# Kernel optimization log

Hardware: AMD Instinct MI355X
Metric: run time of the kernel (lower is better)

Reference implementation:

```python
import jax, jax.numpy as jnp
import numpy as np

B = 65536   # batch
S = 3       # pad_size / seq len
DIN = 72    # input feature dim
D = 100     # dim_model
H = 10      # num_head
DH = D // H # dim_head = 10
FF = 512    # ffn hidden
L = 8       # encoder layers
CLS = 40    # cls_dim


def _pos_encoding():
    pe = np.array([[pos / 10000.0 ** (i // 2 * 2.0 / D) for i in range(D)]
                   for pos in range(S)], dtype=np.float32)
    pe[:, 0::2] = np.sin(pe[:, 0::2])
    pe[:, 1::2] = np.cos(pe[:, 1::2])
    return jnp.asarray(pe)  # [S, D]


def setup_inputs() -> dict:
    key = jax.random.key(0)
    ks = jax.random.split(key, 24)
    n = lambda k, shape: 0.05 * jax.random.normal(k, shape, dtype=jnp.float32)
    inp = {
        'x': jax.random.normal(ks[0], (B, S, DIN), dtype=jnp.float32),
        'label': jax.random.randint(ks[1], (B,), 0, CLS),
        'fa_label': jax.random.randint(ks[2], (B,), 0, CLS),
        'We': n(ks[3], (D, DIN)), 'be': n(ks[4], (D,)),
        'pe': _pos_encoding(),
        'Wq': n(ks[5], (L, D, D)), 'bq': n(ks[6], (L, D)),
        'Wk': n(ks[7], (L, D, D)), 'bk': n(ks[8], (L, D)),
        'Wv': n(ks[9], (L, D, D)), 'bv': n(ks[10], (L, D)),
        'Wo': n(ks[11], (L, D, D)), 'bo': n(ks[12], (L, D)),
        'ln1_g': jnp.ones((L, D), jnp.float32), 'ln1_b': jnp.zeros((L, D), jnp.float32),
        'W1': n(ks[13], (L, FF, D)), 'b1': n(ks[14], (L, FF)),
        'W2': n(ks[15], (L, D, FF)), 'b2': n(ks[16], (L, D)),
        'ln2_g': jnp.ones((L, D), jnp.float32), 'ln2_b': jnp.zeros((L, D), jnp.float32),
        'Wf': n(ks[17], (CLS, S * D)), 'bf': n(ks[18], (CLS,)),
    }
    return inp


def _ln(x, g, b, eps=1e-5):
    m = x.mean(-1, keepdims=True)
    v = ((x - m) ** 2).mean(-1, keepdims=True)
    return (x - m) / jnp.sqrt(v + eps) * g + b


def _forward(x, We, be, pe, Wq, bq, Wk, bk, Wv, bv, Wo, bo,
             ln1_g, ln1_b, W1, b1, W2, b2, ln2_g, ln2_b, Wf, bf):
    Bsz = x.shape[0]
    out = x @ We.T + be          # [B, S, D] embedding
    out = out + pe               # positional encoding (dropout = identity in eval)
    scale = DH ** -0.5
    for i in range(L):
        xin = out
        Q = xin @ Wq[i].T + bq[i]
        K = xin @ Wk[i].T + bk[i]
        V = xin @ Wv[i].T + bv[i]
        # Faithful row-major reshape (original uses .view, which interleaves
        # seq and head dims rather than a transpose-based head split).
        Qh = Q.reshape(Bsz * H, -1, DH)   # [B*H, S, DH]
        Kh = K.reshape(Bsz * H, -1, DH)
        Vh = V.reshape(Bsz * H, -1, DH)
        attn = jax.nn.softmax(jnp.einsum('bqd,bkd->bqk', Qh, Kh) * scale, axis=-1)
        ctx = jnp.einsum('bqk,bkd->bqd', attn, Vh).reshape(Bsz, -1, D)
        out = _ln(ctx @ Wo[i].T + bo[i] + xin, ln1_g[i], ln1_b[i])
        # position-wise FFN
        h = jax.nn.relu(out @ W1[i].T + b1[i])
        out = _ln(h @ W2[i].T + b2[i] + out, ln2_g[i], ln2_b[i])
    out = out.reshape(Bsz, S * D) @ Wf.T + bf   # [B, CLS]
    return out


def reference(x, label, fa_label, We, be, pe, Wq, bq, Wk, bk, Wv, bv, Wo, bo,
              ln1_g, ln1_b, W1, b1, W2, b2, ln2_g, ln2_b, Wf, bf):
    # label / fa_label are unused in the original forward
    return _forward(x, We, be, pe, Wq, bq, Wk, bk, Wv, bv, Wo, bo,
                    ln1_g, ln1_b, W1, b1, W2, b2, ln2_g, ln2_b, Wf, bf)
```

## Files before the change

kernel.cpp:

```cpp
#include <hip/hip_runtime.h>
#include <hip/hip_bf16.h>


typedef __attribute__((ext_vector_type(8))) short short8;
typedef __attribute__((ext_vector_type(4))) float floatx4;

namespace {
constexpr int S = 3, DIN = 72, D = 100, FF = 512, L = 8, CLS = 40;
constexpr int NB = 16, R = 48, NT = 256;
constexpr int LDA = 136;
constexpr int LDH = 200;
constexpr float SCALE = 0.3162277660168379f;

constexpr int PL_QKVO = 7 * 4 * 512;
constexpr int WQ_OFF = 0;
constexpr int WK_OFF = WQ_OFF + L * PL_QKVO;
constexpr int WV_OFF = WK_OFF + L * PL_QKVO;
constexpr int WO_OFF = WV_OFF + L * PL_QKVO;
constexpr int PL_W1 = 32 * 4 * 512;
constexpr int W1_OFF = WO_OFF + L * PL_QKVO;
constexpr int PL_W2 = 7 * 16 * 512;
constexpr int W2_OFF = W1_OFF + L * PL_W1;
constexpr int WE_OFF = W2_OFF + L * PL_W2;
}

__device__ __forceinline__ unsigned short f2bf(float f) {
  unsigned int u = __float_as_uint(f);
  u = u + 0x7fffu + ((u >> 16) & 1u);
  return (unsigned short)(u >> 16);
}

__device__ __forceinline__ unsigned pkbf(float a, float b) {
  __hip_bfloat162 h = __float22bfloat162_rn(make_float2(a, b));
  return *reinterpret_cast<unsigned*>(&h);
}

__device__ __forceinline__ void st_bf4(unsigned short* p, floatx4 v) {
  *reinterpret_cast<uint2*>(p) = make_uint2(pkbf(v.x, v.y), pkbf(v.z, v.w));
}

__device__ __forceinline__ void load10(float* o, const unsigned short* p) {
  const unsigned* u = (const unsigned*)p;
#pragma unroll
  for (int w = 0; w < 5; ++w) {
    unsigned x = u[w];
    o[2 * w] = __uint_as_float(x << 16);
    o[2 * w + 1] = __uint_as_float(x & 0xffff0000u);
  }
}

__device__ __forceinline__ void ldwf4(const unsigned short* base, short8* o) {
#pragma unroll
  for (int ks = 0; ks < 4; ++ks) o[ks] = *(const short8*)(base + ks * 512);
}

__device__ __forceinline__ void ln_rows(float* xrow, const float* srow,
                                        const float* __restrict__ g,
                                        const float* __restrict__ b,
                                        unsigned short* sArow, int ln,
                                        int cnt) {
  floatx4 v[7];
  float sum = 0.f;
#pragma unroll
  for (int i = 0; i < 7; ++i)
    if (i < cnt) {
      const int col = i * 16 + ln * 4;
      floatx4 t = *(const floatx4*)(xrow + col) + *(const floatx4*)(srow + col);
      v[i] = t;
      sum += t.x + t.y + t.z + t.w;
    }
  sum += __shfl_xor(sum, 1, 4);
  sum += __shfl_xor(sum, 2, 4);
  const float mean = sum * 0.01f;
  float var = 0.f;
#pragma unroll
  for (int i = 0; i < 7; ++i)
    if (i < cnt) {
      floatx4 d = v[i] - mean;
      var += d.x * d.x + d.y * d.y + d.z * d.z + d.w * d.w;
    }
  var += __shfl_xor(var, 1, 4);
  var += __shfl_xor(var, 2, 4);
  const float rstd = rsqrtf(var * 0.01f + 1e-5f);
#pragma unroll
  for (int i = 0; i < 7; ++i)
    if (i < cnt) {
      const int col = i * 16 + ln * 4;
      floatx4 o = (v[i] - mean) * rstd * *(const floatx4*)(g + col) +
                  *(const floatx4*)(b + col);
      *(floatx4*)(xrow + col) = o;
      st_bf4(sArow + col, o);
    }
}

__global__ void prep_weights(const float* __restrict__ Wq, const float* __restrict__ Wk,
                             const float* __restrict__ Wv, const float* __restrict__ Wo,
                             const float* __restrict__ W1, const float* __restrict__ W2,
                             const float* __restrict__ We,
                             unsigned short* __restrict__ ws) {
  const int gid = blockIdx.x * 256 + threadIdx.x;
  constexpr int T_QKVO = 8 * 7 * 4 * 64;
  constexpr int T_W1 = 8 * 32 * 4 * 64;
  constexpr int T_W2 = 8 * 7 * 16 * 64;
  constexpr int T_WE = 7 * 3 * 64;
  if (gid >= 4 * T_QKVO + T_W1 + T_W2 + T_WE) return;

  const float* src;
  unsigned short* dst;
  int within, ntc, ksc, N, Ksrc, lstride;
  if (gid < 4 * T_QKVO) {
    const int t = gid / T_QKVO;
    within = gid % T_QKVO;
    src = (t == 0 ? Wq : t == 1 ? Wk : t == 2 ? Wv : Wo);
    dst = ws + (t == 0 ? WQ_OFF : t == 1 ? WK_OFF : t == 2 ? WV_OFF : WO_OFF);
    ntc = 7; ksc = 4; N = 100; Ksrc = 100; lstride = 10000;
  } else if (gid < 4 * T_QKVO + T_W1) {
    within = gid - 4 * T_QKVO;
    src = W1; dst = ws + W1_OFF;
    ntc = 32; ksc = 4; N = 512; Ksrc = 100; lstride = 51200;
  } else if (gid < 4 * T_QKVO + T_W1 + T_W2) {
    within = gid - 4 * T_QKVO - T_W1;
    src = W2; dst = ws + W2_OFF;
    ntc = 7; ksc = 16; N = 100; Ksrc = 512; lstride = 51200;
  } else {
    within = gid - 4 * T_QKVO - T_W1 - T_W2;
    src = We; dst = ws + WE_OFF;
    ntc = 7; ksc = 3; N = 100; Ksrc = 72; lstride = 0;
  }
  const int lane = within & 63;
  int tmp = within >> 6;
  const int ks = tmp % ksc; tmp /= ksc;
  const int nt = tmp % ntc;
  const int lay = tmp / ntc;
  const int n = nt * 16 + (lane & 15);
  const int kb = ks * 32 + (lane >> 4) * 8;
  const float* sp = src + (size_t)lay * lstride + (size_t)n * Ksrc;
  unsigned short o[8];
#pragma unroll
  for (int j = 0; j < 8; ++j) {
    const int k = kb + j;
    float v = (n < N && k < Ksrc) ? sp[k] : 0.f;
    o[j] = f2bf(v);
  }
  uint4 pk = make_uint4((unsigned)o[0] | ((unsigned)o[1] << 16),
                        (unsigned)o[2] | ((unsigned)o[3] << 16),
                        (unsigned)o[4] | ((unsigned)o[5] << 16),
                        (unsigned)o[6] | ((unsigned)o[7] << 16));
  *reinterpret_cast<uint4*>(dst + (size_t)within * 8) = pk;
}

__global__ __launch_bounds__(NT, 3)
void geomap_mfma(const float* __restrict__ gx,
                 const float* __restrict__ be, const float* __restrict__ pe,
                 const float* __restrict__ bq, const float* __restrict__ bk,
                 const float* __restrict__ bv, const float* __restrict__ bo,
                 const float* __restrict__ g1, const float* __restrict__ bt1,
                 const float* __restrict__ b1, const float* __restrict__ b2,
                 const float* __restrict__ g2, const float* __restrict__ bt2,
                 const float* __restrict__ Wf, const float* __restrict__ bfc,
                 const unsigned short* __restrict__ ws,
                 float* __restrict__ gout) {
  __shared__ __align__(16) char smem[51456];
  unsigned short* sA = (unsigned short*)smem;
  float* sXf = (float*)(smem + 13056);
  unsigned short* sQ = (unsigned short*)(smem + 32256);
  unsigned short* sK = (unsigned short*)(smem + 41856);
  float* scr = (float*)(smem + 32256);
  unsigned short* sH = (unsigned short*)(smem + 32256);

  const int tid = threadIdx.x;
  const int lane = tid & 63;
  const int wid = tid >> 6;
  const int l15 = lane & 15;
  const int quad = lane >> 4;
  const int blk = blockIdx.x;

  const int row_o = tid >> 2, ln_o = tid & 3;
  const int cnt_o = (ln_o == 0) ? 7 : 6;

  for (int i = tid; i < R * LDA / 2; i += NT) ((unsigned*)sA)[i] = 0u;
  __syncthreads();
  for (int i = tid; i < R * DIN / 2; i += NT) {
    const int row = i / 36, c = (i % 36) * 2;
    const float2 f2 = *(const float2*)(gx + ((size_t)blk * R + row) * DIN + c);
    ((unsigned*)sA)[row * (LDA / 2) + (c >> 1)] = pkbf(f2.x, f2.y);
  }
  __syncthreads();

  {
    short8 xe[3][3];
#pragma unroll
    for (int mt = 0; mt < 3; ++mt)
#pragma unroll
      for (int ks = 0; ks < 3; ++ks)
        xe[mt][ks] = *(const short8*)(sA + (mt * 16 + l15) * LDA + ks * 32 + quad * 8);
    __syncthreads();
    for (int nt = wid; nt < 7; nt += 4) {
      const unsigned short* wb = ws + WE_OFF + (size_t)(nt * 3) * 512 + (size_t)lane * 8;
      short8 w0 = *(const short8*)(wb);
      short8 w1 = *(const short8*)(wb + 512);
      short8 w2 = *(const short8*)(wb + 1024);
      const int n0 = nt * 16 + quad * 4;
      floatx4 a[3];
#pragma unroll
      for (int mt = 0; mt < 3; ++mt) {
        a[mt] = floatx4{0.f, 0.f, 0.f, 0.f};
        a[mt] = __builtin_amdgcn_mfma_f32_16x16x32_bf16(w0, xe[mt][0], a[mt], 0, 0, 0);
        a[mt] = __builtin_amdgcn_mfma_f32_16x16x32_bf16(w1, xe[mt][1], a[mt], 0, 0, 0);
        a[mt] = __builtin_amdgcn_mfma_f32_16x16x32_bf16(w2, xe[mt][2], a[mt], 0, 0, 0);
      }
      if (n0 < D) {
        const floatx4 bev = *(const floatx4*)(be + n0);
#pragma unroll
        for (int mt = 0; mt < 3; ++mt) {
          const int row = mt * 16 + l15;
          const int s = row % 3;
          const floatx4 pev = *(const floatx4*)(pe + s * D + n0);
          const floatx4 o = a[mt] + bev + pev;
          *(floatx4*)(sXf + row * D + n0) = o;
          st_bf4(sA + row * LDA + n0, o);
        }
      }
    }
  }
  __syncthreads();

  for (int lay = 0; lay < L; ++lay) {
    {
      short8 xf[3][4];
#pragma unroll
      for (int mt = 0; mt < 3; ++mt)
#pragma unroll
        for (int ks = 0; ks < 4; ++ks)
          xf[mt][ks] = *(const short8*)(sA + (mt * 16 + l15) * LDA + ks * 32 + quad * 8);
      __syncthreads();
      const unsigned short* wbase[3] = {ws + WQ_OFF + lay * PL_QKVO,
                                        ws + WK_OFF + lay * PL_QKVO,
                                        ws + WV_OFF + lay * PL_QKVO};
      for (int u = wid; u < 21; u += 4) {
        const int mat = u / 7, nt = u % 7;
        short8 wf[4];
        ldwf4(wbase[mat] + (size_t)nt * 2048 + (size_t)lane * 8, wf);
        const int n0 = nt * 16 + quad * 4;
        floatx4 bias = {0.f, 0.f, 0.f, 0.f};
        const float* bsrc = (mat == 0 ? bq : mat == 1 ? bk : bv) + lay * D;
        if (n0 < D) bias = *(const floatx4*)(bsrc + n0);
        floatx4 a0 = bias, a1 = bias, a2 = bias;
#pragma unroll
        for (int ks = 0; ks < 4; ++ks) {
          a0 = __builtin_amdgcn_mfma_f32_16x16x32_bf16(wf[ks], xf[0][ks], a0, 0, 0, 0);
          a1 = __builtin_amdgcn_mfma_f32_16x16x32_bf16(wf[ks], xf[1][ks], a1, 0, 0, 0);
          a2 = __builtin_amdgcn_mfma_f32_16x16x32_bf16(wf[ks], xf[2][ks], a2, 0, 0, 0);
        }
        if (n0 < D) {
          const floatx4 av[3] = {a0, a1, a2};
#pragma unroll
          for (int mt = 0; mt < 3; ++mt) {
            const int row = mt * 16 + l15;
            if (mat == 0) st_bf4(sQ + row * 100 + n0, av[mt]);
            else if (mat == 1) st_bf4(sK + row * 100 + n0, av[mt]);
            else st_bf4(sA + row * LDA + n0, av[mt]);
          }
        }
      }
    }
    __syncthreads();

    if (tid < 160) {
      const int e = tid / 10, h = tid % 10;
      const unsigned short* Qe = sQ + e * 300;
      const unsigned short* Ke = sK + e * 300;
      float Kv[3][10];
#pragma unroll
      for (int t = 0; t < 3; ++t) load10(Kv[t], Ke + h * 30 + t * 10);
      float p[3][3];
#pragma unroll
      for (int sq = 0; sq < 3; ++sq) {
        float q[10];
        load10(q, Qe + h * 30 + sq * 10);
        float sc[3];
#pragma unroll
        for (int t = 0; t < 3; ++t) {
          float s0 = 0.f;
#pragma unroll
          for (int j = 0; j < 10; ++j) s0 += q[j] * Kv[t][j];
          sc[t] = s0 * SCALE;
        }
        const float m = fmaxf(sc[0], fmaxf(sc[1], sc[2]));
        float p0 = __expf(sc[0] - m), p1 = __expf(sc[1] - m), p2 = __expf(sc[2] - m);
        const float inv = 1.f / (p0 + p1 + p2);
        p[sq][0] = p0 * inv; p[sq][1] = p1 * inv; p[sq][2] = p2 * inv;
      }
      float ctx[3][10];
#pragma unroll
      for (int sq = 0; sq < 3; ++sq)
#pragma unroll
        for (int j = 0; j < 10; ++j) ctx[sq][j] = 0.f;
#pragma unroll
      for (int t = 0; t < 3; ++t) {
        const int pv = h * 30 + t * 10;
        float vv[10];
        load10(vv, sA + (e * 3 + pv / 100) * LDA + (pv % 100));
#pragma unroll
        for (int sq = 0; sq < 3; ++sq)
#pragma unroll
          for (int j = 0; j < 10; ++j) ctx[sq][j] += p[sq][t] * vv[j];
      }
#pragma unroll
      for (int sq = 0; sq < 3; ++sq) {
        const int pq = h * 30 + sq * 10;
        unsigned* dp = (unsigned*)(sA + (e * 3 + pq / 100) * LDA + (pq % 100));
#pragma unroll
        for (int w = 0; w < 5; ++w)
          dp[w] = pkbf(ctx[sq][2 * w], ctx[sq][2 * w + 1]);
      }
    }
    __syncthreads();

    {
      short8 cf[3][4];
#pragma unroll
      for (int mt = 0; mt < 3; ++mt)
#pragma unroll
        for (int ks = 0; ks < 4; ++ks)
          cf[mt][ks] = *(const short8*)(sA + (mt * 16 + l15) * LDA + ks * 32 + quad * 8);
      const unsigned short* wbase = ws + WO_OFF + lay * PL_QKVO;
      for (int u = wid; u < 7; u += 4) {
        short8 wf[4];
        ldwf4(wbase + (size_t)u * 2048 + (size_t)lane * 8, wf);
        const int n0 = u * 16 + quad * 4;
        floatx4 bias = {0.f, 0.f, 0.f, 0.f};
        if (n0 < D) bias = *(const floatx4*)(bo + lay * D + n0);
        floatx4 a0 = bias, a1 = bias, a2 = bias;
#pragma unroll
        for (int ks = 0; ks < 4; ++ks) {
          a0 = __builtin_amdgcn_mfma_f32_16x16x32_bf16(wf[ks], cf[0][ks], a0, 0, 0, 0);
          a1 = __builtin_amdgcn_mfma_f32_16x16x32_bf16(wf[ks], cf[1][ks], a1, 0, 0, 0);
          a2 = __builtin_amdgcn_mfma_f32_16x16x32_bf16(wf[ks], cf[2][ks], a2, 0, 0, 0);
        }
        if (n0 < D) {
          const floatx4 av[3] = {a0, a1, a2};
#pragma unroll
          for (int mt = 0; mt < 3; ++mt)
            *(floatx4*)(scr + (mt * 16 + l15) * D + n0) = av[mt];
        }
      }
    }
    __syncthreads();
    if (tid < 192)
      ln_rows(sXf + row_o * D, scr + row_o * D, g1 + lay * D, bt1 + lay * D,
              sA + row_o * LDA, ln_o, cnt_o);
    __syncthreads();

    {
      short8 ff[3][4];
#pragma unroll
      for (int mt = 0; mt < 3; ++mt)
#pragma unroll
        for (int ks = 0; ks < 4; ++ks)
          ff[mt][ks] = *(const short8*)(sA + (mt * 16 + l15) * LDA + ks * 32 + quad * 8);
      floatx4 facc[2][3];
      const int ntA = wid, ntB = wid + 4;
#pragma unroll
      for (int idx = 0; idx < 2; ++idx) {
        const int nt = idx == 0 ? ntA : ntB;
        const int n0 = nt * 16 + quad * 4;
        floatx4 bias = {0.f, 0.f, 0.f, 0.f};
        if (nt < 7 && n0 < D) bias = *(const floatx4*)(b2 + lay * D + n0);
#pragma unroll
        for (int mt = 0; mt < 3; ++mt) facc[idx][mt] = bias;
      }
      const unsigned short* w1b = ws + W1_OFF + (size_t)lay * PL_W1;
      const unsigned short* w2b = ws + W2_OFF + (size_t)lay * PL_W2;

#pragma unroll
      for (int c = 0; c < 3; ++c) {
        const int base_nt = c * 12;
        const int cnt_nt = (c == 2) ? 8 : 12;
        const int kb = c * 6, ke = kb + ((c == 2) ? 4 : 6);
        for (int l = wid; l < cnt_nt; l += 4) {
          const int ntg = base_nt + l;
          short8 wf[4];
          ldwf4(w1b + (size_t)ntg * 2048 + (size_t)lane * 8, wf);
          const floatx4 b1v = *(const floatx4*)(b1 + lay * FF + ntg * 16 + quad * 4);
          floatx4 a0 = b1v, a1 = b1v, a2 = b1v;
#pragma unroll
          for (int ks = 0; ks < 4; ++ks) {
            a0 = __builtin_amdgcn_mfma_f32_16x16x32_bf16(wf[ks], ff[0][ks], a0, 0, 0, 0);
            a1 = __builtin_amdgcn_mfma_f32_16x16x32_bf16(wf[ks], ff[1][ks], a1, 0, 0, 0);
            a2 = __builtin_amdgcn_mfma_f32_16x16x32_bf16(wf[ks], ff[2][ks], a2, 0, 0, 0);
          }
          const int nloc = l * 16 + quad * 4;
          const floatx4 av[3] = {a0, a1, a2};
#pragma unroll
          for (int mt = 0; mt < 3; ++mt) {
            const int row = mt * 16 + l15;
            floatx4 r;
            r.x = fmaxf(av[mt].x, 0.f); r.y = fmaxf(av[mt].y, 0.f);
            r.z = fmaxf(av[mt].z, 0.f); r.w = fmaxf(av[mt].w, 0.f);
            st_bf4(sH + row * LDH + nloc, r);
          }
        }
        __syncthreads();
        short8 wA = *(const short8*)(w2b + (size_t)(ntA * 16 + kb) * 512 + (size_t)lane * 8);
        short8 wB = wA;
        if (ntB < 7)
          wB = *(const short8*)(w2b + (size_t)(ntB * 16 + kb) * 512 + (size_t)lane * 8);
        for (int ksl = kb; ksl < ke; ++ksl) {
          short8 nA = wA, nB = wB;
          if (ksl + 1 < ke) {
            nA = *(const short8*)(w2b + (size_t)(ntA * 16 + ksl + 1) * 512 + (size_t)lane * 8);
            if (ntB < 7)
              nB = *(const short8*)(w2b + (size_t)(ntB * 16 + ksl + 1) * 512 + (size_t)lane * 8);
          }
          short8 hf[3];
#pragma unroll
          for (int mt = 0; mt < 3; ++mt)
            hf[mt] = *(const short8*)(sH + (mt * 16 + l15) * LDH + (ksl - kb) * 32 + quad * 8);
#pragma unroll
          for (int mt = 0; mt < 3; ++mt)
            facc[0][mt] = __builtin_amdgcn_mfma_f32_16x16x32_bf16(wA, hf[mt], facc[0][mt], 0, 0, 0);
          if (ntB < 7) {
#pragma unroll
            for (int mt = 0; mt < 3; ++mt)
              facc[1][mt] = __builtin_amdgcn_mfma_f32_16x16x32_bf16(wB, hf[mt], facc[1][mt], 0, 0, 0);
          }
          wA = nA; wB = nB;
        }
        __syncthreads();
      }
#pragma unroll
      for (int idx = 0; idx < 2; ++idx) {
        const int nt = idx == 0 ? ntA : ntB;
        const int n0 = nt * 16 + quad * 4;
        if (nt < 7 && n0 < D) {
#pragma unroll
          for (int mt = 0; mt < 3; ++mt)
            *(floatx4*)(scr + (mt * 16 + l15) * D + n0) = facc[idx][mt];
        }
      }
    }
    __syncthreads();
    if (tid < 192)
      ln_rows(sXf + row_o * D, scr + row_o * D, g2 + lay * D, bt2 + lay * D,
              sA + row_o * LDA, ln_o, cnt_o);
    __syncthreads();
  }

  if (tid < 160) {
    const int c = tid % 40, eg = tid / 40;
    float acc[4];
#pragma unroll
    for (int i = 0; i < 4; ++i) acc[i] = bfc[c];
    const floatx4* wr = (const floatx4*)(Wf + c * 300);
    for (int kq = 0; kq < 75; ++kq) {
      const floatx4 w4 = wr[kq];
#pragma unroll
      for (int i = 0; i < 4; ++i) {
        const floatx4 x4 = *(const floatx4*)(sXf + (eg * 4 + i) * 300 + kq * 4);
        acc[i] += w4.x * x4.x + w4.y * x4.y + w4.z * x4.z + w4.w * x4.w;
      }
    }
#pragma unroll
    for (int i = 0; i < 4; ++i)
      gout[((size_t)blk * NB + eg * 4 + i) * CLS + c] = acc[i];
  }
}

extern "C" void kernel_launch(void* const* d_in, const int* in_sizes, int n_in,
                              void* d_out, int out_size, void* d_ws,
                              size_t ws_size, hipStream_t stream) {
  const float* x   = (const float*)d_in[0];
  const float* We  = (const float*)d_in[3];
  const float* be  = (const float*)d_in[4];
  const float* pe  = (const float*)d_in[5];
  const float* Wq  = (const float*)d_in[6];
  const float* bq  = (const float*)d_in[7];
  const float* Wk  = (const float*)d_in[8];
  const float* bk  = (const float*)d_in[9];
  const float* Wv  = (const float*)d_in[10];
  const float* bv  = (const float*)d_in[11];
  const float* Wo  = (const float*)d_in[12];
  const float* bo  = (const float*)d_in[13];
  const float* g1  = (const float*)d_in[14];
  const float* bt1 = (const float*)d_in[15];
  const float* W1  = (const float*)d_in[16];
  const float* b1  = (const float*)d_in[17];
  const float* W2  = (const float*)d_in[18];
  const float* b2  = (const float*)d_in[19];
  const float* g2  = (const float*)d_in[20];
  const float* bt2 = (const float*)d_in[21];
  const float* Wf  = (const float*)d_in[22];
  const float* bf  = (const float*)d_in[23];
  float* out = (float*)d_out;
  unsigned short* ws = (unsigned short*)d_ws;

  prep_weights<<<710, 256, 0, stream>>>(Wq, Wk, Wv, Wo, W1, W2, We, ws);

  const int B = in_sizes[0] / (S * DIN);
  const int blocks = B / NB;
  geomap_mfma<<<blocks, 256, 0, stream>>>(x, be, pe, bq, bk, bv, bo,
                                          g1, bt1, b1, b2, g2, bt2, Wf, bf,
                                          ws, out);
}
```

Measured before the change: 1.370 ms.

## Software-prefetch MFMA weight fragments one tile ahead across all GEMM stages

Weight fragments for the QKV, Wo, W1 GEMMs are now loaded from global memory one iteration ahead into registers (double-buffered), and across stage and layer boundaries (Wo during QKV, W1 during Wo, next layer's Wq during FFN). The aim is to hide global/L2 load latency behind MFMA work and barriers instead of stalling on each tile's load. This raises register pressure (extra short8 buffers), which could lower occupancy or cause spills.

```diff
diff --git a/kernel.cpp b/kernel.cpp
--- a/kernel.cpp
+++ b/kernel.cpp
@@ -52,6 +52,11 @@
 __device__ __forceinline__ void ldwf4(const unsigned short* base, short8* o) {
 #pragma unroll
   for (int ks = 0; ks < 4; ++ks) o[ks] = *(const short8*)(base + ks * 512);
+}
+
+__device__ __forceinline__ void cpwf4(short8* d, const short8* s) {
+#pragma unroll
+  for (int ks = 0; ks < 4; ++ks) d[ks] = s[ks];
 }
 
 __device__ __forceinline__ void ln_rows(float* xrow, const float* srow,
@@ -225,7 +230,15 @@
   }
   __syncthreads();
 
+  short8 wfq[4];
+  ldwf4(ws + WQ_OFF + (size_t)wid * 2048 + (size_t)lane * 8, wfq);
+
   for (int lay = 0; lay < L; ++lay) {
+    const unsigned short* w1b = ws + W1_OFF + (size_t)lay * PL_W1;
+    const unsigned short* w2b = ws + W2_OFF + (size_t)lay * PL_W2;
+    short8 wo_wf[2][4];
+    short8 f1wf[4];
+
     {
       short8 xf[3][4];
 #pragma unroll
@@ -238,9 +251,11 @@
                                         ws + WK_OFF + lay * PL_QKVO,
                                         ws + WV_OFF + lay * PL_QKVO};
       for (int u = wid; u < 21; u += 4) {
+        short8 nwf[4];
+        const bool more = (u + 4 < 21);
+        if (more)
+          ldwf4(wbase[(u + 4) / 7] + (size_t)((u + 4) % 7) * 2048 + (size_t)lane * 8, nwf);
         const int mat = u / 7, nt = u % 7;
-        short8 wf[4];
-        ldwf4(wbase[mat] + (size_t)nt * 2048 + (size_t)lane * 8, wf);
         const int n0 = nt * 16 + quad * 4;
         floatx4 bias = {0.f, 0.f, 0.f, 0.f};
         const float* bsrc = (mat == 0 ? bq : mat == 1 ? bk : bv) + lay * D;
@@ -248,9 +263,9 @@
         floatx4 a0 = bias, a1 = bias, a2 = bias;
 #pragma unroll
         for (int ks = 0; ks < 4; ++ks) {
-          a0 = __builtin_amdgcn_mfma_f32_16x16x32_bf16(wf[ks], xf[0][ks], a0, 0, 0, 0);
-          a1 = __builtin_amdgcn_mfma_f32_16x16x32_bf16(wf[ks], xf[1][ks], a1, 0, 0, 0);
-          a2 = __builtin_amdgcn_mfma_f32_16x16x32_bf16(wf[ks], xf[2][ks], a2, 0, 0, 0);
+          a0 = __builtin_amdgcn_mfma_f32_16x16x32_bf16(wfq[ks], xf[0][ks], a0, 0, 0, 0);
+          a1 = __builtin_amdgcn_mfma_f32_16x16x32_bf16(wfq[ks], xf[1][ks], a1, 0, 0, 0);
+          a2 = __builtin_amdgcn_mfma_f32_16x16x32_bf16(wfq[ks], xf[2][ks], a2, 0, 0, 0);
         }
         if (n0 < D) {
           const floatx4 av[3] = {a0, a1, a2};
@@ -262,6 +277,14 @@
             else st_bf4(sA + row * LDA + n0, av[mt]);
           }
         }
+        if (more) cpwf4(wfq, nwf);
+      }
+#pragma unroll
+      for (int idx = 0; idx < 2; ++idx) {
+        const int u2 = wid + 4 * idx;
+        if (u2 < 7)
+          ldwf4(ws + WO_OFF + lay * PL_QKVO + (size_t)u2 * 2048 + (size_t)lane * 8,
+                wo_wf[idx]);
       }
     }
     __syncthreads();
@@ -324,27 +347,29 @@
 #pragma unroll
         for (int ks = 0; ks < 4; ++ks)
           cf[mt][ks] = *(const short8*)(sA + (mt * 16 + l15) * LDA + ks * 32 + quad * 8);
-      const unsigned short* wbase = ws + WO_OFF + lay * PL_QKVO;
-      for (int u = wid; u < 7; u += 4) {
-        short8 wf[4];
-        ldwf4(wbase + (size_t)u * 2048 + (size_t)lane * 8, wf);
-        const int n0 = u * 16 + quad * 4;
-        floatx4 bias = {0.f, 0.f, 0.f, 0.f};
-        if (n0 < D) bias = *(const floatx4*)(bo + lay * D + n0);
-        floatx4 a0 = bias, a1 = bias, a2 = bias;
-#pragma unroll
-        for (int ks = 0; ks < 4; ++ks) {
-          a0 = __builtin_amdgcn_mfma_f32_16x16x32_bf16(wf[ks], cf[0][ks], a0, 0, 0, 0);
-          a1 = __builtin_amdgcn_mfma_f32_16x16x32_bf16(wf[ks], cf[1][ks], a1, 0, 0, 0);
-          a2 = __builtin_amdgcn_mfma_f32_16x16x32_bf16(wf[ks], cf[2][ks], a2, 0, 0, 0);
-        }
-        if (n0 < D) {
-          const floatx4 av[3] = {a0, a1, a2};
-#pragma unroll
-          for (int mt = 0; mt < 3; ++mt)
-            *(floatx4*)(scr + (mt * 16 + l15) * D + n0) = av[mt];
-        }
-      }
+#pragma unroll
+      for (int idx = 0; idx < 2; ++idx) {
+        const int u = wid + 4 * idx;
+        if (u < 7) {
+          const int n0 = u * 16 + quad * 4;
+          floatx4 bias = {0.f, 0.f, 0.f, 0.f};
+          if (n0 < D) bias = *(const floatx4*)(bo + lay * D + n0);
+          floatx4 a0 = bias, a1 = bias, a2 = bias;
+#pragma unroll
+          for (int ks = 0; ks < 4; ++ks) {
+            a0 = __builtin_amdgcn_mfma_f32_16x16x32_bf16(wo_wf[idx][ks], cf[0][ks], a0, 0, 0, 0);
+            a1 = __builtin_amdgcn_mfma_f32_16x16x32_bf16(wo_wf[idx][ks], cf[1][ks], a1, 0, 0, 0);
+            a2 = __builtin_amdgcn_mfma_f32_16x16x32_bf16(wo_wf[idx][ks], cf[2][ks], a2, 0, 0, 0);
+          }
+          if (n0 < D) {
+            const floatx4 av[3] = {a0, a1, a2};
+#pragma unroll
+            for (int mt = 0; mt < 3; ++mt)
+              *(floatx4*)(scr + (mt * 16 + l15) * D + n0) = av[mt];
+          }
+        }
+      }
+      ldwf4(w1b + (size_t)wid * 2048 + (size_t)lane * 8, f1wf);
     }
     __syncthreads();
     if (tid < 192)
@@ -370,25 +395,28 @@
 #pragma unroll
         for (int mt = 0; mt < 3; ++mt) facc[idx][mt] = bias;
       }
-      const unsigned short* w1b = ws + W1_OFF + (size_t)lay * PL_W1;
-      const unsigned short* w2b = ws + W2_OFF + (size_t)lay * PL_W2;
 
 #pragma unroll
       for (int c = 0; c < 3; ++c) {
         const int base_nt = c * 12;
         const int cnt_nt = (c == 2) ? 8 : 12;
         const int kb = c * 6, ke = kb + ((c == 2) ? 4 : 6);
+        short8 wf1[4];
+        if (c == 0) cpwf4(wf1, f1wf);
+        else ldwf4(w1b + (size_t)(base_nt + wid) * 2048 + (size_t)lane * 8, wf1);
         for (int l = wid; l < cnt_nt; l += 4) {
+          short8 nxt[4];
+          const bool more = (l + 4 < cnt_nt);
+          if (more)
+            ldwf4(w1b + (size_t)(base_nt + l + 4) * 2048 + (size_t)lane * 8, nxt);
           const int ntg = base_nt + l;
-          short8 wf[4];
-          ldwf4(w1b + (size_t)ntg * 2048 + (size_t)lane * 8, wf);
           const floatx4 b1v = *(const floatx4*)(b1 + lay * FF + ntg * 16 + quad * 4);
           floatx4 a0 = b1v, a1 = b1v, a2 = b1v;
 #pragma unroll
           for (int ks = 0; ks < 4; ++ks) {
-            a0 = __builtin_amdgcn_mfma_f32_16x16x32_bf16(wf[ks], ff[0][ks], a0, 0, 0, 0);
-            a1 = __builtin_amdgcn_mfma_f32_16x16x32_bf16(wf[ks], ff[1][ks], a1, 0, 0, 0);
-            a2 = __builtin_amdgcn_mfma_f32_16x16x32_bf16(wf[ks], ff[2][ks], a2, 0, 0, 0);
+            a0 = __builtin_amdgcn_mfma_f32_16x16x32_bf16(wf1[ks], ff[0][ks], a0, 0, 0, 0);
+            a1 = __builtin_amdgcn_mfma_f32_16x16x32_bf16(wf1[ks], ff[1][ks], a1, 0, 0, 0);
+            a2 = __builtin_amdgcn_mfma_f32_16x16x32_bf16(wf1[ks], ff[2][ks], a2, 0, 0, 0);
           }
           const int nloc = l * 16 + quad * 4;
           const floatx4 av[3] = {a0, a1, a2};
@@ -400,6 +428,7 @@
             r.z = fmaxf(av[mt].z, 0.f); r.w = fmaxf(av[mt].w, 0.f);
             st_bf4(sH + row * LDH + nloc, r);
           }
+          if (more) cpwf4(wf1, nxt);
         }
         __syncthreads();
         short8 wA = *(const short8*)(w2b + (size_t)(ntA * 16 + kb) * 512 + (size_t)lane * 8);
@@ -439,6 +468,9 @@
             *(floatx4*)(scr + (mt * 16 + l15) * D + n0) = facc[idx][mt];
         }
       }
+      if (lay + 1 < L)
+        ldwf4(ws + WQ_OFF + (lay + 1) * PL_QKVO + (size_t)wid * 2048 + (size_t)lane * 8,
+              wfq);
     }
     __syncthreads();
     if (tid < 192)
```

New measurement: 2.633 ms. 1.92x slower.
